# Kernel tuning notes

Hardware: AMD Instinct MI355X
Metric: run time of the kernel (lower is better)

Reference implementation:

```python
import jax, jax.numpy as jnp
import numpy as np

EMBED_DIM = 1024
NUM_HEADS = 16
HEAD_DIM = EMBED_DIM // NUM_HEADS
BATCH, SEQ = 1, 4096


def setup_inputs() -> dict:
    key = jax.random.key(0)
    k1, k2, k3 = jax.random.split(key, 3)
    hidden_states = jax.random.normal(k1, (BATCH, SEQ, EMBED_DIM), dtype=jnp.float32)
    W_qkv = jax.random.normal(k2, (3 * EMBED_DIM, EMBED_DIM), dtype=jnp.float32) * 0.02
    b_qkv = jnp.zeros((3 * EMBED_DIM,), dtype=jnp.float32)
    # torch init: identity per head, perturb slightly to make test non-trivial
    eye = jnp.broadcast_to(jnp.eye(HEAD_DIM, dtype=jnp.float32), (NUM_HEADS, HEAD_DIM, HEAD_DIM))
    hebbian_trace = eye + 0.01 * jax.random.normal(k3, (NUM_HEADS, HEAD_DIM, HEAD_DIM), dtype=jnp.float32)
    return {"hidden_states": hidden_states, "W_qkv": W_qkv, "b_qkv": b_qkv, "hebbian_trace": hebbian_trace}


def reference(hidden_states, W_qkv, b_qkv, hebbian_trace):
    B, S, E = hidden_states.shape
    H, D = NUM_HEADS, HEAD_DIM
    qkv = hidden_states @ W_qkv.T + b_qkv              # [B,S,3E]
    q, k, v = jnp.split(qkv, 3, axis=-1)
    # [B,H,S,D]
    q = q.reshape(B, S, H, D).transpose(0, 2, 1, 3)
    k = k.reshape(B, S, H, D).transpose(0, 2, 1, 3)
    v = v.reshape(B, S, H, D).transpose(0, 2, 1, 3)
    scores = jnp.einsum('bhqd,bhkd->bhqk', q, k) / jnp.sqrt(jnp.float32(D))
    attn = jax.nn.softmax(scores, axis=-1)
    weighted_v = jnp.einsum('bhqk,bhkd->bhqd', attn, v)  # [B,H,S,D]
    # torch einsum 'blhd,hdd->blhd': repeated 'd' in trace -> diagonal scaling
    wv = weighted_v.transpose(0, 2, 1, 3)               # [B,S,H,D]
    v_transformed = jnp.einsum('blhd,hdd->blhd', wv, hebbian_trace)
    return v_transformed.reshape(B, S, E)
```

## Files before the change

### kernel.cpp

```cpp
#include <hip/hip_runtime.h>
#include <hip/hip_bf16.h>
#include <stdint.h>

#define S_LEN 4096

typedef short s16x8  __attribute__((ext_vector_type(8)));
typedef float f32x4  __attribute__((ext_vector_type(4)));
typedef float f32x16 __attribute__((ext_vector_type(16)));

#define CEXP 0.18033688011112042f

__device__ __forceinline__ unsigned short f2bf(float f) {
    union { float f; unsigned u; } v; v.f = f;
    unsigned r = v.u + 0x7fffu + ((v.u >> 16) & 1u);
    return (unsigned short)(r >> 16);
}

__device__ __forceinline__ ushort2 pkbf(float a, float b) {
    float2 f; f.x = a; f.y = b;
    __hip_bfloat162 h = __float22bfloat162_rn(f);
    union { __hip_bfloat162 h; ushort2 u; } cv; cv.h = h;
    return cv.u;
}

__device__ __forceinline__ ushort4 pkbf4(float x, float y, float z, float w) {
    ushort2 lo = pkbf(x, y), hi = pkbf(z, w);
    ushort4 r; r.x = lo.x; r.y = lo.y; r.z = hi.x; r.w = hi.y;
    return r;
}

typedef const __attribute__((address_space(1))) void* gas_t;
typedef __attribute__((address_space(3))) void* sas_t;

__device__ __forceinline__ void async16(const void* g, void* s) {
    __builtin_amdgcn_global_load_lds((gas_t)g, (sas_t)s, 16, 0, 0);
}

__global__ __launch_bounds__(256) void cvt_bf16(
    const float* __restrict__ X, const float* __restrict__ W,
    unsigned short* __restrict__ Xb, unsigned short* __restrict__ Wb)
{
    const long NX = 4194304;
    long i = (long)(blockIdx.x * 256 + threadIdx.x) * 8;
    const float* src; unsigned short* dst; long off;
    if (i < NX) { src = X; dst = Xb; off = i; }
    else        { src = W; dst = Wb; off = i - NX; }
    float4 a = *(const float4*)(src + off);
    float4 b = *(const float4*)(src + off + 4);
    union { s16x8 v; ushort4 q[2]; } o;
    o.q[0] = pkbf4(a.x, a.y, a.z, a.w);
    o.q[1] = pkbf4(b.x, b.y, b.z, b.w);
    *(s16x8*)(dst + off) = o.v;
}

__global__ __launch_bounds__(256) void qkv_gemm_bf16(
    const unsigned short* __restrict__ Xb, const unsigned short* __restrict__ Wb,
    const float* __restrict__ bias,
    unsigned short* __restrict__ Qb, unsigned short* __restrict__ Kb,
    unsigned short* __restrict__ Vt)
{
    __shared__ __align__(16) unsigned short sm[17408];
    unsigned short* As = sm;
    unsigned short* Bs = sm + 8192;

    const int t = threadIdx.x;
    const int l = t & 63;
    const int w = t >> 6;
    const int bm = blockIdx.y, bn = blockIdx.x;
    const int rowBase = (w >> 1) * 64;
    const int colBase = (w & 1) * 64;

    f32x4 acc[4][4];
#pragma unroll
    for (int i = 0; i < 4; i++)
#pragma unroll
        for (int j = 0; j < 4; j++) acc[i][j] = (f32x4)0.f;

    const int srow = l >> 3;
    const int scol = (l & 7) * 8;

    for (int kt = 0; kt < 16; ++kt) {
        const int k0 = kt * 64;
#pragma unroll
        for (int c = 0; c < 4; ++c) {
            int m = w * 4 + c;
            const unsigned short* ga = Xb + (bm * 128 + m * 8 + srow) * 1024 + k0 + scol;
            const unsigned short* gb = Wb + (bn * 128 + m * 8 + srow) * 1024 + k0 + scol;
            async16(ga, As + m * 512);
            async16(gb, Bs + m * 512);
        }
        __syncthreads();

#pragma unroll
        for (int kc = 0; kc < 2; ++kc) {
            s16x8 af[4], bf[4];
#pragma unroll
            for (int i = 0; i < 4; i++) {
                af[i] = *(const s16x8*)(As + (rowBase + i * 16 + (l & 15)) * 64 + kc * 32 + (l >> 4) * 8);
                bf[i] = *(const s16x8*)(Bs + (colBase + i * 16 + (l & 15)) * 64 + kc * 32 + (l >> 4) * 8);
            }
#pragma unroll
            for (int i = 0; i < 4; i++)
#pragma unroll
                for (int j = 0; j < 4; j++)
                    acc[i][j] = __builtin_amdgcn_mfma_f32_16x16x32_bf16(af[i], bf[j], acc[i][j], 0, 0, 0);
        }
        __syncthreads();
    }

    if (bn < 16) {
#pragma unroll
        for (int j = 0; j < 4; j++) {
            int col = bn * 128 + colBase + j * 16 + (l & 15);
            float bv = bias[col];
            int region = col >> 10;
            int within = col & 1023;
            int h = within >> 6, d = within & 63;
            unsigned short* dst = (region == 0) ? Qb : Kb;
            float scl = (region == 0) ? CEXP : 1.0f;
#pragma unroll
            for (int i = 0; i < 4; i++) {
                int s0 = bm * 128 + rowBase + i * 16 + ((l >> 4) << 2);
#pragma unroll
                for (int r = 0; r < 4; r++)
                    dst[(h * S_LEN + s0 + r) * 64 + d] = f2bf((acc[i][j][r] + bv) * scl);
            }
        }
    } else {
        __syncthreads();
        unsigned short* Lt = sm;
#pragma unroll
        for (int j = 0; j < 4; j++) {
            int cl = colBase + j * 16 + (l & 15);
            float bv = bias[bn * 128 + cl];
#pragma unroll
            for (int i = 0; i < 4; i++) {
                int s0 = rowBase + i * 16 + ((l >> 4) << 2);
                *(ushort4*)(Lt + cl * 136 + s0) =
                    pkbf4(acc[i][j][0] + bv, acc[i][j][1] + bv,
                          acc[i][j][2] + bv, acc[i][j][3] + bv);
            }
        }
        __syncthreads();
#pragma unroll
        for (int p = 0; p < 8; ++p) {
            int dl  = (t >> 4) + p * 16;
            int sch = (t & 15) * 8;
            int o = bn * 128 + dl - 2048;
            int h = o >> 6, d = o & 63;
            s16x8 v = *(const s16x8*)(Lt + dl * 136 + sch);
            *(s16x8*)(Vt + (h * 64 + d) * S_LEN + bm * 128 + sch) = v;
        }
    }
}

__global__ __launch_bounds__(256) void qkv_gemm_f32(
    const float* __restrict__ X, const float* __restrict__ W,
    const float* __restrict__ bias,
    unsigned short* __restrict__ Qb, unsigned short* __restrict__ Kb,
    unsigned short* __restrict__ Vt)
{
    __shared__ __align__(16) unsigned short sm[17408];
    unsigned short* As = sm;
    unsigned short* Bs = sm + 5120;

    const int t = threadIdx.x;
    const int l = t & 63;
    const int w = t >> 6;
    const int bm = blockIdx.y, bn = blockIdx.x;
    const int rowBase = (w >> 1) * 64;
    const int colBase = (w & 1) * 64;

    f32x4 acc[4][4];
#pragma unroll
    for (int i = 0; i < 4; i++)
#pragma unroll
        for (int j = 0; j < 4; j++) acc[i][j] = (f32x4)0.f;

    const int sr = t >> 3;
    const int sc = (t & 7) * 4;

    for (int kt = 0; kt < 32; ++kt) {
        const int k0 = kt * 32;
#pragma unroll
        for (int p = 0; p < 4; ++p) {
            int r = sr + p * 32;
            float4 xa = *(const float4*)(X + (bm * 128 + r) * 1024 + k0 + sc);
            float4 wb = *(const float4*)(W + (bn * 128 + r) * 1024 + k0 + sc);
            *(ushort4*)(As + r * 40 + sc) = pkbf4(xa.x, xa.y, xa.z, xa.w);
            *(ushort4*)(Bs + r * 40 + sc) = pkbf4(wb.x, wb.y, wb.z, wb.w);
        }
        __syncthreads();

        s16x8 af[4], bf[4];
#pragma unroll
        for (int i = 0; i < 4; i++) {
            af[i] = *(const s16x8*)(As + (rowBase + i * 16 + (l & 15)) * 40 + (l >> 4) * 8);
            bf[i] = *(const s16x8*)(Bs + (colBase + i * 16 + (l & 15)) * 40 + (l >> 4) * 8);
        }
#pragma unroll
        for (int i = 0; i < 4; i++)
#pragma unroll
            for (int j = 0; j < 4; j++)
                acc[i][j] = __builtin_amdgcn_mfma_f32_16x16x32_bf16(af[i], bf[j], acc[i][j], 0, 0, 0);
        __syncthreads();
    }

    if (bn < 16) {
#pragma unroll
        for (int j = 0; j < 4; j++) {
            int col = bn * 128 + colBase + j * 16 + (l & 15);
            float bv = bias[col];
            int region = col >> 10;
            int within = col & 1023;
            int h = within >> 6, d = within & 63;
            unsigned short* dst = (region == 0) ? Qb : Kb;
            float scl = (region == 0) ? CEXP : 1.0f;
#pragma unroll
            for (int i = 0; i < 4; i++) {
                int s0 = bm * 128 + rowBase + i * 16 + ((l >> 4) << 2);
#pragma unroll
                for (int r = 0; r < 4; r++)
                    dst[(h * S_LEN + s0 + r) * 64 + d] = f2bf((acc[i][j][r] + bv) * scl);
            }
        }
    } else {
        __syncthreads();
        unsigned short* Lt = sm;
#pragma unroll
        for (int j = 0; j < 4; j++) {
            int cl = colBase + j * 16 + (l & 15);
            float bv = bias[bn * 128 + cl];
#pragma unroll
            for (int i = 0; i < 4; i++) {
                int s0 = rowBase + i * 16 + ((l >> 4) << 2);
                *(ushort4*)(Lt + cl * 136 + s0) =
                    pkbf4(acc[i][j][0] + bv, acc[i][j][1] + bv,
                          acc[i][j][2] + bv, acc[i][j][3] + bv);
            }
        }
        __syncthreads();
#pragma unroll
        for (int p = 0; p < 8; ++p) {
            int dl  = (t >> 4) + p * 16;
            int sch = (t & 15) * 8;
            int o = bn * 128 + dl - 2048;
            int h = o >> 6, d = o & 63;
            s16x8 v = *(const s16x8*)(Lt + dl * 136 + sch);
            *(s16x8*)(Vt + (h * 64 + d) * S_LEN + bm * 128 + sch) = v;
        }
    }
}

__global__ __launch_bounds__(256) void attn(
    const unsigned short* __restrict__ Qb, const unsigned short* __restrict__ Kb,
    const unsigned short* __restrict__ Vt, const float* __restrict__ trace,
    float* __restrict__ out)
{
    __shared__ __align__(16) unsigned short sm[17920];
    __shared__ float tdiag[64];
    unsigned short* Ks  = sm;
    unsigned short* Vts = sm + 4608;
    unsigned short* Ps  = sm + 9216;

    const int t = threadIdx.x;
    const int l = t & 63;
    const int w = t >> 6;
    const int h = blockIdx.y;
    const int qbase = blockIdx.x * 128 + w * 32;
    const int l31 = l & 31;
    const int lh  = l >> 5;

    if (t < 64) tdiag[t] = trace[h * 4096 + t * 65];

    s16x8 qf[4];
#pragma unroll
    for (int ks = 0; ks < 4; ks++)
        qf[ks] = *(const s16x8*)(Qb + (h * S_LEN + qbase + l31) * 64 + ks * 16 + lh * 8);

    f32x16 O0 = (f32x16)0.f, O1 = (f32x16)0.f;
    float lp0 = 0.f, lp1 = 0.f, lp2 = 0.f, lp3 = 0.f;

    const int strow = t >> 2;
    const int stch  = (t & 3) * 16;

    unsigned short* Pw = Ps + w * 2176 + l31 * 68;

    for (int kt = 0; kt < 64; ++kt) {
        const int kv0 = kt * 64;
        {
            const unsigned short* ksrc = Kb + (h * S_LEN + kv0 + strow) * 64 + stch;
            const unsigned short* vsrc = Vt + (h * 64 + strow) * S_LEN + kv0 + stch;
            s16x8 k0v = *(const s16x8*)(ksrc);
            s16x8 k1v = *(const s16x8*)(ksrc + 8);
            s16x8 v0v = *(const s16x8*)(vsrc);
            s16x8 v1v = *(const s16x8*)(vsrc + 8);
            *(s16x8*)(Ks  + strow * 72 + stch)     = k0v;
            *(s16x8*)(Ks  + strow * 72 + stch + 8) = k1v;
            *(s16x8*)(Vts + strow * 72 + stch)     = v0v;
            *(s16x8*)(Vts + strow * 72 + stch + 8) = v1v;
        }
        __syncthreads();

        f32x16 S0 = (f32x16)0.f, S1 = (f32x16)0.f;
#pragma unroll
        for (int ks = 0; ks < 4; ks++) {
            s16x8 a0 = *(const s16x8*)(Ks + l31 * 72 + ks * 16 + lh * 8);
            s16x8 a1 = *(const s16x8*)(Ks + (32 + l31) * 72 + ks * 16 + lh * 8);
            S0 = __builtin_amdgcn_mfma_f32_32x32x16_bf16(a0, qf[ks], S0, 0, 0, 0);
            S1 = __builtin_amdgcn_mfma_f32_32x32x16_bf16(a1, qf[ks], S1, 0, 0, 0);
        }

#pragma unroll
        for (int i = 0; i < 16; i += 4) {
            float p0 = __builtin_amdgcn_exp2f(S0[i+0]); S0[i+0] = p0; lp0 += p0;
            float p1 = __builtin_amdgcn_exp2f(S0[i+1]); S0[i+1] = p1; lp1 += p1;
            float p2 = __builtin_amdgcn_exp2f(S0[i+2]); S0[i+2] = p2; lp2 += p2;
            float p3 = __builtin_amdgcn_exp2f(S0[i+3]); S0[i+3] = p3; lp3 += p3;
        }
#pragma unroll
        for (int i = 0; i < 16; i += 4) {
            float p0 = __builtin_amdgcn_exp2f(S1[i+0]); S1[i+0] = p0; lp0 += p0;
            float p1 = __builtin_amdgcn_exp2f(S1[i+1]); S1[i+1] = p1; lp1 += p1;
            float p2 = __builtin_amdgcn_exp2f(S1[i+2]); S1[i+2] = p2; lp2 += p2;
            float p3 = __builtin_amdgcn_exp2f(S1[i+3]); S1[i+3] = p3; lp3 += p3;
        }

#pragma unroll
        for (int g = 0; g < 4; ++g) {
            *(ushort4*)(Pw + g * 8 + lh * 4)      = pkbf4(S0[g*4], S0[g*4+1], S0[g*4+2], S0[g*4+3]);
            *(ushort4*)(Pw + 32 + g * 8 + lh * 4) = pkbf4(S1[g*4], S1[g*4+1], S1[g*4+2], S1[g*4+3]);
        }

#pragma unroll
        for (int ks = 0; ks < 4; ks++) {
            union { s16x8 v; ushort4 q[2]; } pu;
            pu.q[0] = *(const ushort4*)(Pw + ks * 16 + lh * 8);
            pu.q[1] = *(const ushort4*)(Pw + ks * 16 + lh * 8 + 4);
            s16x8 av0 = *(const s16x8*)(Vts + l31 * 72 + ks * 16 + lh * 8);
            s16x8 av1 = *(const s16x8*)(Vts + (32 + l31) * 72 + ks * 16 + lh * 8);
            O0 = __builtin_amdgcn_mfma_f32_32x32x16_bf16(av0, pu.v, O0, 0, 0, 0);
            O1 = __builtin_amdgcn_mfma_f32_32x32x16_bf16(av1, pu.v, O1, 0, 0, 0);
        }
        __syncthreads();
    }

    float l_part = (lp0 + lp1) + (lp2 + lp3);
    float l_tot = l_part + __shfl_xor(l_part, 32);
    float inv_l = 1.f / l_tot;

    __syncthreads();
    float* Lo = (float*)sm + w * 2176;
#pragma unroll
    for (int dt = 0; dt < 2; ++dt) {
        const f32x16& Ox = dt ? O1 : O0;
#pragma unroll
        for (int g = 0; g < 4; ++g) {
            int d0 = dt * 32 + g * 8 + lh * 4;
            float4 vv;
            vv.x = Ox[g*4+0] * inv_l * tdiag[d0+0];
            vv.y = Ox[g*4+1] * inv_l * tdiag[d0+1];
            vv.z = Ox[g*4+2] * inv_l * tdiag[d0+2];
            vv.w = Ox[g*4+3] * inv_l * tdiag[d0+3];
            *(float4*)(Lo + l31 * 68 + d0) = vv;
        }
    }
    __syncthreads();
#pragma unroll
    for (int it = 0; it < 8; ++it) {
        int ql = it * 4 + (l >> 4);
        float4 vv = *(const float4*)(Lo + ql * 68 + (l & 15) * 4);
        *(float4*)(out + (qbase + ql) * 1024 + h * 64 + (l & 15) * 4) = vv;
    }
}

extern "C" void kernel_launch(void* const* d_in, const int* in_sizes, int n_in,
                              void* d_out, int out_size, void* d_ws, size_t ws_size,
                              hipStream_t stream) {
    const float* X     = (const float*)d_in[0];
    const float* W     = (const float*)d_in[1];
    const float* bias  = (const float*)d_in[2];
    const float* trace = (const float*)d_in[3];
    float* out = (float*)d_out;

    unsigned short* Qb = (unsigned short*)d_ws;
    unsigned short* Kb = Qb + 4194304;
    unsigned short* Vt = Kb + 4194304;
    unsigned short* Xb = Vt + 4194304;
    unsigned short* Wb = Xb + 4194304;

    const size_t NEED = (size_t)(4194304 * 4 + 3145728) * 2;

    if (ws_size >= NEED) {
        cvt_bf16<<<3584, 256, 0, stream>>>(X, W, Xb, Wb);
        qkv_gemm_bf16<<<dim3(24, 32), 256, 0, stream>>>(Xb, Wb, bias, Qb, Kb, Vt);
    } else {
        qkv_gemm_f32<<<dim3(24, 32), 256, 0, stream>>>(X, W, bias, Qb, Kb, Vt);
    }
    attn<<<dim3(32, 16), 256, 0, stream>>>(Qb, Kb, Vt, trace, out);
}
```

Baseline: 228.8 us.

## Split attention KV range across two blocks with atomic merge and XCD-aware remap

The attention kernel now splits each head's KV sequence into two halves handled by separate blocks. This doubles the grid so more blocks are resident per CU. Partial outputs and row sums are combined with float atomics into a zeroed output and a workspace buffer, and a new norm_out kernel applies the 1/l normalization and the trace diagonal scaling. Both the GEMM and the attention kernel remap their 1D block index so neighbouring tiles share an XCD, and attention gets a min-blocks launch bound. The costs are two memsets, an extra kernel pass over the output, and atomic traffic on a 16 MB output.

```diff
diff --git a/kernel.cpp b/kernel.cpp
--- a/kernel.cpp
+++ b/kernel.cpp
@@ -66,7 +66,11 @@
     const int t = threadIdx.x;
     const int l = t & 63;
     const int w = t >> 6;
-    const int bm = blockIdx.y, bn = blockIdx.x;
+    const int bid = blockIdx.x;
+    const int xcd = bid & 7;
+    const int ii  = bid >> 3;
+    const int bn  = 3 * xcd + (ii % 3);
+    const int bm  = ii / 3;
     const int rowBase = (w >> 1) * 64;
     const int colBase = (w & 1) * 64;
 
@@ -252,13 +256,12 @@
     }
 }
 
-__global__ __launch_bounds__(256) void attn(
+__global__ __launch_bounds__(256, 4) void attn(
     const unsigned short* __restrict__ Qb, const unsigned short* __restrict__ Kb,
-    const unsigned short* __restrict__ Vt, const float* __restrict__ trace,
-    float* __restrict__ out)
+    const unsigned short* __restrict__ Vt,
+    float* __restrict__ out, float* __restrict__ lsum)
 {
     __shared__ __align__(16) unsigned short sm[17920];
-    __shared__ float tdiag[64];
     unsigned short* Ks  = sm;
     unsigned short* Vts = sm + 4608;
     unsigned short* Ps  = sm + 9216;
@@ -266,13 +269,17 @@
     const int t = threadIdx.x;
     const int l = t & 63;
     const int w = t >> 6;
-    const int h = blockIdx.y;
-    const int qbase = blockIdx.x * 128 + w * 32;
+    const int bid = blockIdx.x;
+    const int xcd = bid & 7;
+    const int ii  = bid >> 3;
+    const int combo = xcd * 4 + (ii & 3);
+    const int h   = combo >> 1;
+    const int kvs = combo & 1;
+    const int qbk = ii >> 2;
+    const int qbase = qbk * 128 + w * 32;
     const int l31 = l & 31;
     const int lh  = l >> 5;
 
-    if (t < 64) tdiag[t] = trace[h * 4096 + t * 65];
-
     s16x8 qf[4];
 #pragma unroll
     for (int ks = 0; ks < 4; ks++)
@@ -286,8 +293,8 @@
 
     unsigned short* Pw = Ps + w * 2176 + l31 * 68;
 
-    for (int kt = 0; kt < 64; ++kt) {
-        const int kv0 = kt * 64;
+    for (int kt = 0; kt < 32; ++kt) {
+        const int kv0 = kvs * 2048 + kt * 64;
         {
             const unsigned short* ksrc = Kb + (h * S_LEN + kv0 + strow) * 64 + stch;
             const unsigned short* vsrc = Vt + (h * 64 + strow) * S_LEN + kv0 + stch;
@@ -347,7 +354,7 @@
 
     float l_part = (lp0 + lp1) + (lp2 + lp3);
     float l_tot = l_part + __shfl_xor(l_part, 32);
-    float inv_l = 1.f / l_tot;
+    if (lh == 0) atomicAdd(lsum + h * S_LEN + qbase + l31, l_tot);
 
     __syncthreads();
     float* Lo = (float*)sm + w * 2176;
@@ -358,10 +365,7 @@
         for (int g = 0; g < 4; ++g) {
             int d0 = dt * 32 + g * 8 + lh * 4;
             float4 vv;
-            vv.x = Ox[g*4+0] * inv_l * tdiag[d0+0];
-            vv.y = Ox[g*4+1] * inv_l * tdiag[d0+1];
-            vv.z = Ox[g*4+2] * inv_l * tdiag[d0+2];
-            vv.w = Ox[g*4+3] * inv_l * tdiag[d0+3];
+            vv.x = Ox[g*4+0]; vv.y = Ox[g*4+1]; vv.z = Ox[g*4+2]; vv.w = Ox[g*4+3];
             *(float4*)(Lo + l31 * 68 + d0) = vv;
         }
     }
@@ -370,8 +374,30 @@
     for (int it = 0; it < 8; ++it) {
         int ql = it * 4 + (l >> 4);
         float4 vv = *(const float4*)(Lo + ql * 68 + (l & 15) * 4);
-        *(float4*)(out + (qbase + ql) * 1024 + h * 64 + (l & 15) * 4) = vv;
-    }
+        float* dst = out + (qbase + ql) * 1024 + h * 64 + (l & 15) * 4;
+        atomicAdd(dst + 0, vv.x);
+        atomicAdd(dst + 1, vv.y);
+        atomicAdd(dst + 2, vv.z);
+        atomicAdd(dst + 3, vv.w);
+    }
+}
+
+__global__ __launch_bounds__(256) void norm_out(
+    float* __restrict__ out, const float* __restrict__ lsum,
+    const float* __restrict__ trace)
+{
+    int g = blockIdx.x * 256 + threadIdx.x;
+    int base = g * 4;
+    int s = base >> 10;
+    int e = base & 1023;
+    int h = e >> 6, d0 = e & 63;
+    float invl = 1.0f / lsum[h * S_LEN + s];
+    float4 v = *(float4*)(out + base);
+    v.x *= invl * trace[h * 4096 + (d0 + 0) * 65];
+    v.y *= invl * trace[h * 4096 + (d0 + 1) * 65];
+    v.z *= invl * trace[h * 4096 + (d0 + 2) * 65];
+    v.w *= invl * trace[h * 4096 + (d0 + 3) * 65];
+    *(float4*)(out + base) = v;
 }
 
 extern "C" void kernel_launch(void* const* d_in, const int* in_sizes, int n_in,
@@ -386,16 +412,23 @@
     unsigned short* Qb = (unsigned short*)d_ws;
     unsigned short* Kb = Qb + 4194304;
     unsigned short* Vt = Kb + 4194304;
-    unsigned short* Xb = Vt + 4194304;
+    float*          ls = (float*)(Vt + 4194304);
+    unsigned short* Xb = (unsigned short*)(ls + 65536);
     unsigned short* Wb = Xb + 4194304;
 
-    const size_t NEED = (size_t)(4194304 * 4 + 3145728) * 2;
-
-    if (ws_size >= NEED) {
+    const size_t NEED_BF16 = (size_t)3 * 8388608 + 262144 + 8388608 + 6291456;
+    const size_t NEED_F32  = (size_t)3 * 8388608 + 262144;
+
+    hipMemsetAsync(d_out, 0, (size_t)out_size * 4, stream);
+    hipMemsetAsync(ls, 0, 65536 * 4, stream);
+
+    if (ws_size >= NEED_BF16) {
         cvt_bf16<<<3584, 256, 0, stream>>>(X, W, Xb, Wb);
-        qkv_gemm_bf16<<<dim3(24, 32), 256, 0, stream>>>(Xb, Wb, bias, Qb, Kb, Vt);
+        qkv_gemm_bf16<<<768, 256, 0, stream>>>(Xb, Wb, bias, Qb, Kb, Vt);
     } else {
+        (void)NEED_F32;
         qkv_gemm_f32<<<dim3(24, 32), 256, 0, stream>>>(X, W, bias, Qb, Kb, Vt);
     }
-    attn<<<dim3(32, 16), 256, 0, stream>>>(Qb, Kb, Vt, trace, out);
-}
+    attn<<<1024, 256, 0, stream>>>(Qb, Kb, Vt, out, ls);
+    norm_out<<<4096, 256, 0, stream>>>(out, ls, trace);
+}
```

Measured after the change: 307.6 us. 34.4% more time.

## Split attention KV range across two wave groups and fold trace into V

Applied to the files above, without the earlier changes.

The attention block grows to 512 threads. Two groups of four waves each process half of the key/value sequence for the same 128 queries, and the partial outputs and row sums are combined through shared memory at the end. The per-head diagonal trace scaling moves into the V epilogue of the QKV GEMM, so attention no longer loads or applies it. This doubles the waves available per block to hide latency. The cost is more shared memory (about 72KB) and an extra reduction pass, and applying trace before the bf16 rounding of V changes rounding slightly.

```diff
diff --git a/kernel.cpp b/kernel.cpp
--- a/kernel.cpp
+++ b/kernel.cpp
@@ -55,7 +55,7 @@
 
 __global__ __launch_bounds__(256) void qkv_gemm_bf16(
     const unsigned short* __restrict__ Xb, const unsigned short* __restrict__ Wb,
-    const float* __restrict__ bias,
+    const float* __restrict__ bias, const float* __restrict__ trace,
     unsigned short* __restrict__ Qb, unsigned short* __restrict__ Kb,
     unsigned short* __restrict__ Vt)
 {
@@ -132,13 +132,15 @@
 #pragma unroll
         for (int j = 0; j < 4; j++) {
             int cl = colBase + j * 16 + (l & 15);
+            int o  = bn * 128 + cl - 2048;
             float bv = bias[bn * 128 + cl];
+            float tr = trace[(o >> 6) * 4096 + (o & 63) * 65];
 #pragma unroll
             for (int i = 0; i < 4; i++) {
                 int s0 = rowBase + i * 16 + ((l >> 4) << 2);
                 *(ushort4*)(Lt + cl * 136 + s0) =
-                    pkbf4(acc[i][j][0] + bv, acc[i][j][1] + bv,
-                          acc[i][j][2] + bv, acc[i][j][3] + bv);
+                    pkbf4((acc[i][j][0] + bv) * tr, (acc[i][j][1] + bv) * tr,
+                          (acc[i][j][2] + bv) * tr, (acc[i][j][3] + bv) * tr);
             }
         }
         __syncthreads();
@@ -156,7 +158,7 @@
 
 __global__ __launch_bounds__(256) void qkv_gemm_f32(
     const float* __restrict__ X, const float* __restrict__ W,
-    const float* __restrict__ bias,
+    const float* __restrict__ bias, const float* __restrict__ trace,
     unsigned short* __restrict__ Qb, unsigned short* __restrict__ Kb,
     unsigned short* __restrict__ Vt)
 {
@@ -230,13 +232,15 @@
 #pragma unroll
         for (int j = 0; j < 4; j++) {
             int cl = colBase + j * 16 + (l & 15);
+            int o  = bn * 128 + cl - 2048;
             float bv = bias[bn * 128 + cl];
+            float tr = trace[(o >> 6) * 4096 + (o & 63) * 65];
 #pragma unroll
             for (int i = 0; i < 4; i++) {
                 int s0 = rowBase + i * 16 + ((l >> 4) << 2);
                 *(ushort4*)(Lt + cl * 136 + s0) =
-                    pkbf4(acc[i][j][0] + bv, acc[i][j][1] + bv,
-                          acc[i][j][2] + bv, acc[i][j][3] + bv);
+                    pkbf4((acc[i][j][0] + bv) * tr, (acc[i][j][1] + bv) * tr,
+                          (acc[i][j][2] + bv) * tr, (acc[i][j][3] + bv) * tr);
             }
         }
         __syncthreads();
@@ -252,26 +256,26 @@
     }
 }
 
-__global__ __launch_bounds__(256) void attn(
+__global__ __launch_bounds__(512, 4) void attn(
     const unsigned short* __restrict__ Qb, const unsigned short* __restrict__ Kb,
-    const unsigned short* __restrict__ Vt, const float* __restrict__ trace,
-    float* __restrict__ out)
+    const unsigned short* __restrict__ Vt, float* __restrict__ out)
 {
-    __shared__ __align__(16) unsigned short sm[17920];
-    __shared__ float tdiag[64];
-    unsigned short* Ks  = sm;
-    unsigned short* Vts = sm + 4608;
-    unsigned short* Ps  = sm + 9216;
+    __shared__ __align__(16) unsigned short sm[35840];
+    __shared__ float lArr[256];
 
     const int t = threadIdx.x;
     const int l = t & 63;
     const int w = t >> 6;
+    const int g = w >> 2;
+    const int wq = w & 3;
     const int h = blockIdx.y;
-    const int qbase = blockIdx.x * 128 + w * 32;
+    const int qbase = blockIdx.x * 128 + wq * 32;
     const int l31 = l & 31;
     const int lh  = l >> 5;
 
-    if (t < 64) tdiag[t] = trace[h * 4096 + t * 65];
+    unsigned short* Ks  = sm + g * 9216;
+    unsigned short* Vts = sm + g * 9216 + 4608;
+    unsigned short* Pw  = sm + 18432 + w * 2176 + l31 * 68;
 
     s16x8 qf[4];
 #pragma unroll
@@ -281,13 +285,12 @@
     f32x16 O0 = (f32x16)0.f, O1 = (f32x16)0.f;
     float lp0 = 0.f, lp1 = 0.f, lp2 = 0.f, lp3 = 0.f;
 
-    const int strow = t >> 2;
-    const int stch  = (t & 3) * 16;
-
-    unsigned short* Pw = Ps + w * 2176 + l31 * 68;
-
-    for (int kt = 0; kt < 64; ++kt) {
-        const int kv0 = kt * 64;
+    const int tg    = t & 255;
+    const int strow = tg >> 2;
+    const int stch  = (tg & 3) * 16;
+
+    for (int kt = 0; kt < 32; ++kt) {
+        const int kv0 = g * 2048 + kt * 64;
         {
             const unsigned short* ksrc = Kb + (h * S_LEN + kv0 + strow) * 64 + stch;
             const unsigned short* vsrc = Vt + (h * 64 + strow) * S_LEN + kv0 + stch;
@@ -327,9 +330,9 @@
         }
 
 #pragma unroll
-        for (int g = 0; g < 4; ++g) {
-            *(ushort4*)(Pw + g * 8 + lh * 4)      = pkbf4(S0[g*4], S0[g*4+1], S0[g*4+2], S0[g*4+3]);
-            *(ushort4*)(Pw + 32 + g * 8 + lh * 4) = pkbf4(S1[g*4], S1[g*4+1], S1[g*4+2], S1[g*4+3]);
+        for (int gq = 0; gq < 4; ++gq) {
+            *(ushort4*)(Pw + gq * 8 + lh * 4)      = pkbf4(S0[gq*4], S0[gq*4+1], S0[gq*4+2], S0[gq*4+3]);
+            *(ushort4*)(Pw + 32 + gq * 8 + lh * 4) = pkbf4(S1[gq*4], S1[gq*4+1], S1[gq*4+2], S1[gq*4+3]);
         }
 
 #pragma unroll
@@ -347,30 +350,38 @@
 
     float l_part = (lp0 + lp1) + (lp2 + lp3);
     float l_tot = l_part + __shfl_xor(l_part, 32);
-    float inv_l = 1.f / l_tot;
-
-    __syncthreads();
+    if (lh == 0) lArr[w * 32 + l31] = l_tot;
+
     float* Lo = (float*)sm + w * 2176;
 #pragma unroll
     for (int dt = 0; dt < 2; ++dt) {
         const f32x16& Ox = dt ? O1 : O0;
 #pragma unroll
-        for (int g = 0; g < 4; ++g) {
-            int d0 = dt * 32 + g * 8 + lh * 4;
+        for (int gq = 0; gq < 4; ++gq) {
+            int d0 = dt * 32 + gq * 8 + lh * 4;
             float4 vv;
-            vv.x = Ox[g*4+0] * inv_l * tdiag[d0+0];
-            vv.y = Ox[g*4+1] * inv_l * tdiag[d0+1];
-            vv.z = Ox[g*4+2] * inv_l * tdiag[d0+2];
-            vv.w = Ox[g*4+3] * inv_l * tdiag[d0+3];
+            vv.x = Ox[gq*4+0]; vv.y = Ox[gq*4+1]; vv.z = Ox[gq*4+2]; vv.w = Ox[gq*4+3];
             *(float4*)(Lo + l31 * 68 + d0) = vv;
         }
     }
     __syncthreads();
-#pragma unroll
-    for (int it = 0; it < 8; ++it) {
-        int ql = it * 4 + (l >> 4);
-        float4 vv = *(const float4*)(Lo + ql * 68 + (l & 15) * 4);
-        *(float4*)(out + (qbase + ql) * 1024 + h * 64 + (l & 15) * 4) = vv;
+
+    if (w < 4) {
+        const float* LoA = (float*)sm + w * 2176;
+        const float* LoB = (float*)sm + (w + 4) * 2176;
+#pragma unroll
+        for (int it = 0; it < 8; ++it) {
+            int ql = it * 4 + (l >> 4);
+            float invl = 1.0f / (lArr[w * 32 + ql] + lArr[(w + 4) * 32 + ql]);
+            float4 a = *(const float4*)(LoA + ql * 68 + (l & 15) * 4);
+            float4 b = *(const float4*)(LoB + ql * 68 + (l & 15) * 4);
+            float4 vv;
+            vv.x = (a.x + b.x) * invl;
+            vv.y = (a.y + b.y) * invl;
+            vv.z = (a.z + b.z) * invl;
+            vv.w = (a.w + b.w) * invl;
+            *(float4*)(out + (blockIdx.x * 128 + w * 32 + ql) * 1024 + h * 64 + (l & 15) * 4) = vv;
+        }
     }
 }
 
@@ -389,13 +400,13 @@
     unsigned short* Xb = Vt + 4194304;
     unsigned short* Wb = Xb + 4194304;
 
-    const size_t NEED = (size_t)(4194304 * 4 + 3145728) * 2;
-
-    if (ws_size >= NEED) {
+    const size_t NEED_BF16 = (size_t)3 * 8388608 + 8388608 + 6291456;
+
+    if (ws_size >= NEED_BF16) {
         cvt_bf16<<<3584, 256, 0, stream>>>(X, W, Xb, Wb);
-        qkv_gemm_bf16<<<dim3(24, 32), 256, 0, stream>>>(Xb, Wb, bias, Qb, Kb, Vt);
+        qkv_gemm_bf16<<<dim3(24, 32), 256, 0, stream>>>(Xb, Wb, bias, trace, Qb, Kb, Vt);
     } else {
-        qkv_gemm_f32<<<dim3(24, 32), 256, 0, stream>>>(X, W, bias, Qb, Kb, Vt);
-    }
-    attn<<<dim3(32, 16), 256, 0, stream>>>(Qb, Kb, Vt, trace, out);
-}
+        qkv_gemm_f32<<<dim3(24, 32), 256, 0, stream>>>(X, W, bias, trace, Qb, Kb, Vt);
+    }
+    attn<<<dim3(32, 16), 512, 0, stream>>>(Qb, Kb, Vt, out);
+}
```

Result: faster. 213.3 us (-6.8%).
